# Kernel optimization log

Hardware: AMD Instinct MI355X
Metric: run time of the kernel (lower is better)

The kernel has to match this reference:

```python
import jax, jax.numpy as jnp
import numpy as np

N_AGT = 65536
N_CTX = 65536
E = 400000
D_AGT = 128
D_CTX = 128
EPS = 1e-5


def gn(x, w, b):
    # GroupNorm with num_groups=1 over channel dim of [N, C]
    m = jnp.mean(x, axis=-1, keepdims=True)
    v = jnp.mean((x - m) ** 2, axis=-1, keepdims=True)
    return (x - m) * jax.lax.rsqrt(v + EPS) * w + b


def setup_inputs() -> dict:
    key = jax.random.key(0)
    ks = jax.random.split(key, 24)
    s = 0.05
    inp = {
        "agts": jax.random.normal(ks[0], (N_AGT, D_AGT), jnp.float32),
        "ctx": jax.random.normal(ks[1], (N_CTX, D_CTX), jnp.float32),
        "agt_ctrs": jax.random.normal(ks[2], (N_AGT, 2), jnp.float32),
        "ctx_ctrs": jax.random.normal(ks[3], (N_CTX, 2), jnp.float32),
        "hi": jax.random.randint(ks[4], (E,), 0, N_AGT),
        "wi": jax.random.randint(ks[5], (E,), 0, N_CTX),
        # dist: Linear(2, n_ctx) + bias, ReLU, Linear(n_ctx, n_ctx) GN ng=1
        "dist_w1": jax.random.normal(ks[6], (2, D_CTX), jnp.float32) * s,
        "dist_b1": jnp.zeros((D_CTX,), jnp.float32),
        "dist_w2": jax.random.normal(ks[7], (D_CTX, D_CTX), jnp.float32) * s,
        "dist_gw": jnp.ones((D_CTX,), jnp.float32),
        "dist_gb": jnp.zeros((D_CTX,), jnp.float32),
        # query: Linear(n_agt, n_ctx) GN ng=1
        "q_w": jax.random.normal(ks[8], (D_AGT, D_CTX), jnp.float32) * s,
        "q_gw": jnp.ones((D_CTX,), jnp.float32),
        "q_gb": jnp.zeros((D_CTX,), jnp.float32),
        # ctx: Linear(3*n_ctx, n_agt) GN, then Linear(n_agt, n_agt, bias=False)
        "ctx_w1": jax.random.normal(ks[9], (3 * D_CTX, D_AGT), jnp.float32) * s,
        "ctx_gw": jnp.ones((D_AGT,), jnp.float32),
        "ctx_gb": jnp.zeros((D_AGT,), jnp.float32),
        "ctx_w2": jax.random.normal(ks[10], (D_AGT, D_AGT), jnp.float32) * s,
        # agt: Linear(n_agt, n_agt, bias=False)
        "agt_w": jax.random.normal(ks[11], (D_AGT, D_AGT), jnp.float32) * s,
        # norm: GroupNorm(1, n_agt)
        "norm_w": jnp.ones((D_AGT,), jnp.float32),
        "norm_b": jnp.zeros((D_AGT,), jnp.float32),
        # linear: Linear(n_agt, n_agt) GN, act=False
        "lin_w": jax.random.normal(ks[12], (D_AGT, D_AGT), jnp.float32) * s,
        "lin_gw": jnp.ones((D_AGT,), jnp.float32),
        "lin_gb": jnp.zeros((D_AGT,), jnp.float32),
    }
    return inp


def reference(agts, ctx, agt_ctrs, ctx_ctrs, hi, wi,
              dist_w1, dist_b1, dist_w2, dist_gw, dist_gb,
              q_w, q_gw, q_gb,
              ctx_w1, ctx_gw, ctx_gb, ctx_w2,
              agt_w, norm_w, norm_b,
              lin_w, lin_gw, lin_gb):
    res = agts
    # edge features: relative displacement -> dist MLP
    d = agt_ctrs[hi] - ctx_ctrs[wi]                      # [E, 2]
    d = jax.nn.relu(d @ dist_w1 + dist_b1)               # [E, D_CTX]
    d = jax.nn.relu(gn(d @ dist_w2, dist_gw, dist_gb))
    # query from gathered agent features
    q = jax.nn.relu(gn(agts[hi] @ q_w, q_gw, q_gb))      # [E, D_CTX]
    # gathered context features
    c = ctx[wi]                                          # [E, D_CTX]
    m = jnp.concatenate([d, q, c], axis=1)               # [E, 3*D_CTX]
    m = jax.nn.relu(gn(m @ ctx_w1, ctx_gw, ctx_gb))      # [E, D_AGT]
    m = m @ ctx_w2                                       # [E, D_AGT]
    # aggregate messages back to agents (scatter-add)
    out = agts @ agt_w
    out = out.at[hi].add(m)
    out = jax.nn.relu(gn(out, norm_w, norm_b))
    out = gn(out @ lin_w, lin_gw, lin_gb)                # act=False
    out = jax.nn.relu(out + res)
    return out
```

## Files before the change

kernel.cpp:

```cpp
#include <hip/hip_runtime.h>
#include <hip/hip_bf16.h>

#define TILE_E 32
#define WSTRIDE 132
#define SB 136
#define SF 132
#define FS 16384

#define FRAG_DW2 0
#define FRAG_W1D 1
#define FRAG_CW2 2
#define FRAG_AGT 3
#define FRAG_QW  4
#define FRAG_W1Q 5
#define FRAG_W1C 6
#define FRAG_LIN 7

typedef __attribute__((ext_vector_type(8))) short short8;
typedef __attribute__((ext_vector_type(4))) float f32x4;

__device__ __forceinline__ unsigned short f2bf(float f) {
    union { float f; unsigned u; } v; v.f = f;
    unsigned r = v.u + 0x7fff + ((v.u >> 16) & 1);
    return (unsigned short)(r >> 16);
}

__device__ __forceinline__ float bf2f(unsigned short u) {
    union { unsigned v; float f; } x; x.v = ((unsigned)u) << 16; return x.f;
}

__device__ __forceinline__ f32x4 mfma16(short8 a, short8 b, f32x4 c) {
    return __builtin_amdgcn_mfma_f32_16x16x32_bf16(a, b, c, 0, 0, 0);
}

__device__ __forceinline__ void load_bfrags_fast(const unsigned short* __restrict__ F,
                                                 int wv, int lane, short8 wB[2][4])
{
#pragma unroll
    for (int cb = 0; cb < 2; ++cb)
#pragma unroll
    for (int kc = 0; kc < 4; ++kc)
        wB[cb][kc] = *(const short8*)(F + ((((wv * 2 + cb) * 4 + kc) * 64 + lane) << 3));
}

__device__ __forceinline__ void mfma_gemm32(const unsigned short* __restrict__ X,
                                            const short8 wB[2][4],
                                            f32x4 acc[2][2], int lane)
{
    const int r  = lane & 15;
    const int kg = (lane >> 4) & 3;
#pragma unroll
    for (int rb = 0; rb < 2; ++rb) {
        const unsigned short* xp = X + (rb * 16 + r) * SB + kg * 8;
#pragma unroll
        for (int kc = 0; kc < 4; ++kc) {
            short8 a = *(const short8*)(xp + kc * 32);
            acc[rb][0] = mfma16(a, wB[0][kc], acc[rb][0]);
            acc[rb][1] = mfma16(a, wB[1][kc], acc[rb][1]);
        }
    }
}

__device__ __forceinline__ void gn_row_to_bf16(const float* __restrict__ sY,
                                               const float* __restrict__ gw,
                                               const float* __restrict__ gb,
                                               unsigned short* __restrict__ dst,
                                               int r8, int c0)
{
    const float* yp = sY + r8 * SF + c0;
    float vals[16]; float s1 = 0.f, s2 = 0.f;
#pragma unroll
    for (int i = 0; i < 16; ++i) { float v = yp[i]; vals[i] = v; s1 += v; s2 += v * v; }
#pragma unroll
    for (int off = 4; off >= 1; off >>= 1) {
        s1 += __shfl_xor(s1, off);
        s2 += __shfl_xor(s2, off);
    }
    float m   = s1 * (1.f / 128.f);
    float var = fmaxf(s2 * (1.f / 128.f) - m * m, 0.f);
    float isc = rsqrtf(var + 1e-5f);
    unsigned short* dp = dst + r8 * SB + c0;
#pragma unroll
    for (int i = 0; i < 16; ++i) {
        float y = fmaxf((vals[i] - m) * isc * gw[c0 + i] + gb[c0 + i], 0.f);
        dp[i] = f2bf(y);
    }
}

__device__ __forceinline__ void gn_bf_to_bf16(const unsigned short* __restrict__ sYb,
                                              const float* __restrict__ gw,
                                              const float* __restrict__ gb,
                                              unsigned short* __restrict__ dst,
                                              int r8, int c0)
{
    const unsigned short* yp = sYb + r8 * SB + c0;
    float vals[16]; float s1 = 0.f, s2 = 0.f;
#pragma unroll
    for (int i = 0; i < 16; ++i) { float v = bf2f(yp[i]); vals[i] = v; s1 += v; s2 += v * v; }
#pragma unroll
    for (int off = 4; off >= 1; off >>= 1) {
        s1 += __shfl_xor(s1, off);
        s2 += __shfl_xor(s2, off);
    }
    float m   = s1 * (1.f / 128.f);
    float var = fmaxf(s2 * (1.f / 128.f) - m * m, 0.f);
    float isc = rsqrtf(var + 1e-5f);
    unsigned short* dp = dst + r8 * SB + c0;
#pragma unroll
    for (int i = 0; i < 16; ++i) {
        float y = fmaxf((vals[i] - m) * isc * gw[c0 + i] + gb[c0 + i], 0.f);
        dp[i] = f2bf(y);
    }
}

__global__ __launch_bounds__(256) void prep_hist_kernel(
    const float* __restrict__ W0, const float* __restrict__ W1,
    const float* __restrict__ W2, const float* __restrict__ W3,
    const float* __restrict__ W4, const float* __restrict__ W5,
    const float* __restrict__ W6, const float* __restrict__ W7,
    unsigned short* __restrict__ dst,
    const int* __restrict__ hi, int* __restrict__ hist, int E)
{
    const int b = blockIdx.x;
    if (b < 512) {
        int t = b * 256 + threadIdx.x;
        int m = t >> 14;
        int e = t & (FS - 1);
        int j    = e & 7;
        int lane = (e >> 3) & 63;
        int kc   = (e >> 9) & 3;
        int cb   = (e >> 11) & 1;
        int wv   = (e >> 12) & 3;
        int k = kc * 32 + ((lane >> 4) & 3) * 8 + j;
        int c = wv * 32 + cb * 16 + (lane & 15);
        const float* W = m == 0 ? W0 : m == 1 ? W1 : m == 2 ? W2 : m == 3 ? W3
                       : m == 4 ? W4 : m == 5 ? W5 : m == 6 ? W6 : W7;
        dst[t] = f2bf(W[k * 128 + c]);
    } else {
        for (int i = (b - 512) * 256 + threadIdx.x; i < E; i += 256 * 256)
            atomicAdd(&hist[hi[i]], 1);
    }
}

__device__ __forceinline__ void chunk_sum_body(const int* __restrict__ hist,
                                               int* __restrict__ csum,
                                               int b, int nbins)
{
    __shared__ int red[4];
    int idx = b * 256 + threadIdx.x;
    int v = (idx < nbins) ? hist[idx] : 0;
#pragma unroll
    for (int off = 32; off >= 1; off >>= 1) v += __shfl_xor(v, off);
    if ((threadIdx.x & 63) == 0) red[threadIdx.x >> 6] = v;
    __syncthreads();
    if (threadIdx.x == 0) csum[b] = red[0] + red[1] + red[2] + red[3];
}

__global__ __launch_bounds__(256) void scanB_kernel(const int* __restrict__ csum,
                                                    int* __restrict__ coff, int nchunks)
{
    __shared__ int part[256];
    int t = threadIdx.x;
    int v = (t < nchunks) ? csum[t] : 0;
    part[t] = v;
    __syncthreads();
    for (int off = 1; off < 256; off <<= 1) {
        int p = (t >= off) ? part[t - off] : 0;
        __syncthreads();
        part[t] += p;
        __syncthreads();
    }
    if (t < nchunks) coff[t] = part[t] - v;
}

__global__ __launch_bounds__(256) void scanC_kernel(const int* __restrict__ hist,
                                                    const int* __restrict__ coff,
                                                    int* __restrict__ binCtr, int nbins)
{
    __shared__ int part[256];
    int b = blockIdx.x, t = threadIdx.x;
    int idx = b * 256 + t;
    int v = (idx < nbins) ? hist[idx] : 0;
    part[t] = v;
    __syncthreads();
    for (int off = 1; off < 256; off <<= 1) {
        int p = (t >= off) ? part[t - off] : 0;
        __syncthreads();
        part[t] += p;
        __syncthreads();
    }
    if (idx < nbins) binCtr[idx] = part[t] - v + coff[b];
}

__global__ __launch_bounds__(256) void scatter_kernel(
    const int* __restrict__ hi, const int* __restrict__ wi,
    const float* __restrict__ agt_ctrs, const float* __restrict__ ctx_ctrs,
    int* __restrict__ binCtr,
    int* __restrict__ hiS, int* __restrict__ wiS,
    float* __restrict__ dxS, float* __restrict__ dyS, int E)
{
    for (int i = blockIdx.x * 256 + threadIdx.x; i < E; i += 256 * 256) {
        int h = hi[i], w = wi[i];
        int p = atomicAdd(&binCtr[h], 1);
        hiS[p] = h; wiS[p] = w;
        dxS[p] = agt_ctrs[2 * h]     - ctx_ctrs[2 * w];
        dyS[p] = agt_ctrs[2 * h + 1] - ctx_ctrs[2 * w + 1];
    }
}

__device__ __forceinline__ void kq_tile_body(
    int tile, const float* __restrict__ agts,
    const float* __restrict__ q_gw, const float* __restrict__ q_gb,
    const unsigned short* __restrict__ frags,
    float* __restrict__ qm, int N,
    unsigned short* sX, float* sY, float* sGw, float* sGb)
{
    const int tid  = threadIdx.x;
    const int lane = tid & 63;
    const int wv   = tid >> 6;
    const int colbase = wv * 32;
    const int r8 = tid >> 3, c0 = (tid & 7) * 16;
    const int cl = lane & 15, rq = lane >> 4;

    short8 wBq[2][4], wB1[2][4];
    load_bfrags_fast(frags + FRAG_QW  * FS, wv, lane, wBq);
    load_bfrags_fast(frags + FRAG_W1Q * FS, wv, lane, wB1);
    if (tid < 128) { sGw[tid] = q_gw[tid]; sGb[tid] = q_gb[tid]; }

    const int base = tile * 32;
    {
        int row = base + r8; if (row >= N) row = N - 1;
        const float* src = agts + (size_t)row * 128 + c0;
        short8 v0, v1;
#pragma unroll
        for (int i = 0; i < 8; ++i) { v0[i] = (short)f2bf(src[i]); v1[i] = (short)f2bf(src[i + 8]); }
        short8* dp = (short8*)(sX + r8 * SB + c0);
        dp[0] = v0; dp[1] = v1;
    }
    __syncthreads();

    f32x4 aQ[2][2] = {{{0,0,0,0},{0,0,0,0}},{{0,0,0,0},{0,0,0,0}}};
    mfma_gemm32(sX, wBq, aQ, lane);
    {
#pragma unroll
        for (int rb = 0; rb < 2; ++rb)
#pragma unroll
        for (int cb = 0; cb < 2; ++cb)
#pragma unroll
        for (int q = 0; q < 4; ++q)
            sY[(rb * 16 + rq * 4 + q) * SF + colbase + cb * 16 + cl] = aQ[rb][cb][q];
    }
    __syncthreads();
    gn_row_to_bf16(sY, sGw, sGb, sX, r8, c0);
    __syncthreads();

    f32x4 aM[2][2] = {{{0,0,0,0},{0,0,0,0}},{{0,0,0,0},{0,0,0,0}}};
    mfma_gemm32(sX, wB1, aM, lane);
#pragma unroll
    for (int rb = 0; rb < 2; ++rb)
#pragma unroll
    for (int q = 0; q < 4; ++q) {
        int row = base + rb * 16 + rq * 4 + q;
        if (row < N) {
            float2 v = make_float2(aM[rb][0][q], aM[rb][1][q]);
            *(float2*)(qm + (size_t)row * 128 + colbase + cl * 2) = v;
        }
    }
}

__device__ __forceinline__ void kc_tile_body(
    int tile, const float* __restrict__ ctx,
    const unsigned short* __restrict__ frags,
    float* __restrict__ cm, int N, unsigned short* sX)
{
    const int tid  = threadIdx.x;
    const int lane = tid & 63;
    const int wv   = tid >> 6;
    const int colbase = wv * 32;
    const int r8 = tid >> 3, c0 = (tid & 7) * 16;
    const int cl = lane & 15, rq = lane >> 4;

    short8 wB[2][4];
    load_bfrags_fast(frags + FRAG_W1C * FS, wv, lane, wB);

    const int base = tile * 32;
    {
        int row = base + r8; if (row >= N) row = N - 1;
        const float* src = ctx + (size_t)row * 128 + c0;
        short8 v0, v1;
#pragma unroll
        for (int i = 0; i < 8; ++i) { v0[i] = (short)f2bf(src[i]); v1[i] = (short)f2bf(src[i + 8]); }
        short8* dp = (short8*)(sX + r8 * SB + c0);
        dp[0] = v0; dp[1] = v1;
    }
    __syncthreads();

    f32x4 acc[2][2] = {{{0,0,0,0},{0,0,0,0}},{{0,0,0,0},{0,0,0,0}}};
    mfma_gemm32(sX, wB, acc, lane);
#pragma unroll
    for (int rb = 0; rb < 2; ++rb)
#pragma unroll
    for (int q = 0; q < 4; ++q) {
        int row = base + rb * 16 + rq * 4 + q;
        if (row < N) {
            float2 v = make_float2(acc[rb][0][q], acc[rb][1][q]);
            *(float2*)(cm + (size_t)row * 128 + colbase + cl * 2) = v;
        }
    }
}

__global__ __launch_bounds__(256) void nodes_kernel(
    const int* __restrict__ hist, int* __restrict__ csum,
    const float* __restrict__ agts, const float* __restrict__ ctx,
    const float* __restrict__ q_gw, const float* __restrict__ q_gb,
    const unsigned short* __restrict__ frags,
    float* __restrict__ qm, float* __restrict__ cm,
    int N, int NC, int nchunks, int tilesA)
{
    __shared__ __align__(16) unsigned short sX[32 * SB];
    __shared__ __align__(16) float sY[32 * SF];
    __shared__ float sGw[128], sGb[128];

    const int b = blockIdx.x;
    if (b < nchunks) { chunk_sum_body(hist, csum, b, N); return; }
    int t = b - nchunks;
    if (t < tilesA)
        kq_tile_body(t, agts, q_gw, q_gb, frags, qm, N, sX, sY, sGw, sGb);
    else
        kc_tile_body(t - tilesA, ctx, frags, cm, NC, sX);
}

__global__ __launch_bounds__(256, 3) void edge_sorted_kernel(
    const int* __restrict__ hiS, const int* __restrict__ wiS,
    const float* __restrict__ dxS, const float* __restrict__ dyS,
    const float* __restrict__ dist_w1, const float* __restrict__ dist_b1,
    const float* __restrict__ dist_gw, const float* __restrict__ dist_gb,
    const float* __restrict__ ctx_gw, const float* __restrict__ ctx_gb,
    const unsigned short* __restrict__ frags,
    const float* __restrict__ qm, const float* __restrict__ cm,
    float* __restrict__ msum, int E, int numTiles)
{
    __shared__ __align__(16) unsigned short sH[32 * SB];
    __shared__ __align__(16) unsigned short sYb[32 * SB];
    __shared__ float sW1[3][128];
    __shared__ float sDGw[128], sDGb[128], sCGw[128], sCGb[128];
    __shared__ int sHiA[32], sWiA[32], sKey[33];
    __shared__ float sDx[32], sDy[32];

    const int tid  = threadIdx.x;
    const int lane = tid & 63;
    const int wv   = tid >> 6;
    const int colbase = wv * 32;
    const int r8 = tid >> 3, c0 = (tid & 7) * 16;
    const int cl = lane & 15, rq = lane >> 4;

    short8 wBh[2][4], wBd[2][4];
    load_bfrags_fast(frags + FRAG_DW2 * FS, wv, lane, wBh);
    load_bfrags_fast(frags + FRAG_W1D * FS, wv, lane, wBd);
    if (tid < 128) {
        sW1[0][tid] = dist_w1[tid];
        sW1[1][tid] = dist_w1[128 + tid];
        sW1[2][tid] = dist_b1[tid];
        sDGw[tid] = dist_gw[tid]; sDGb[tid] = dist_gb[tid];
        sCGw[tid] = ctx_gw[tid];  sCGb[tid] = ctx_gb[tid];
    }

    int ph = 0, pw = 0, pkey = -1; float pdx = 0.f, pdy = 0.f;
    if (tid < 32) {
        pkey = -1 - tid;
        int e = blockIdx.x * 32 + tid;
        if (e < E) { ph = hiS[e]; pw = wiS[e]; pkey = ph; pdx = dxS[e]; pdy = dyS[e]; }
    }

    for (int tile = blockIdx.x; tile < numTiles; tile += gridDim.x) {
        __syncthreads();
        if (tid < 32) {
            sHiA[tid] = ph; sWiA[tid] = pw; sKey[tid] = pkey;
            sDx[tid] = pdx; sDy[tid] = pdy;
        }
        __syncthreads();

        if (tid < 32) {
            pkey = -1 - tid; ph = 0; pw = 0; pdx = 0.f; pdy = 0.f;
            int tn = tile + gridDim.x;
            if (tn < numTiles) {
                int e = tn * 32 + tid;
                if (e < E) { ph = hiS[e]; pw = wiS[e]; pkey = ph; pdx = dxS[e]; pdy = dyS[e]; }
            }
        }

        float2 gq[2][4], gc[2][4];
#pragma unroll
        for (int rb = 0; rb < 2; ++rb)
#pragma unroll
        for (int q = 0; q < 4; ++q) {
            int r = rb * 16 + rq * 4 + q;
            gq[rb][q] = *(const float2*)(qm + (size_t)sHiA[r] * 128 + colbase + cl * 2);
            gc[rb][q] = *(const float2*)(cm + (size_t)sWiA[r] * 128 + colbase + cl * 2);
        }

        {
            float dx = sDx[r8], dy = sDy[r8];
            unsigned short* dst = sH + r8 * SB + c0;
#pragma unroll
            for (int i = 0; i < 16; ++i) {
                int c = c0 + i;
                float v = fmaf(dx, sW1[0][c], fmaf(dy, sW1[1][c], sW1[2][c]));
                dst[i] = f2bf(fmaxf(v, 0.f));
            }
        }
        __syncthreads();

        f32x4 acc[2][2] = {{{0,0,0,0},{0,0,0,0}},{{0,0,0,0},{0,0,0,0}}};
        mfma_gemm32(sH, wBh, acc, lane);
        {
#pragma unroll
            for (int rb = 0; rb < 2; ++rb)
#pragma unroll
            for (int cb = 0; cb < 2; ++cb)
#pragma unroll
            for (int q = 0; q < 4; ++q)
                sYb[(rb * 16 + rq * 4 + q) * SB + colbase + cb * 16 + cl] = f2bf(acc[rb][cb][q]);
        }
        __syncthreads();
        gn_bf_to_bf16(sYb, sDGw, sDGb, sH, r8, c0);
        __syncthreads();

        f32x4 a2[2][2];
#pragma unroll
        for (int rb = 0; rb < 2; ++rb)
#pragma unroll
        for (int q = 0; q < 4; ++q) {
            a2[rb][0][q] = gq[rb][q].x + gc[rb][q].x;
            a2[rb][1][q] = gq[rb][q].y + gc[rb][q].y;
        }
        mfma_gemm32(sH, wBd, a2, lane);
        {
#pragma unroll
            for (int rb = 0; rb < 2; ++rb)
#pragma unroll
            for (int cb = 0; cb < 2; ++cb)
#pragma unroll
            for (int q = 0; q < 4; ++q)
                sYb[(rb * 16 + rq * 4 + q) * SB + colbase + cb * 16 + cl] = f2bf(a2[rb][cb][q]);
        }
        __syncthreads();
        gn_bf_to_bf16(sYb, sCGw, sCGb, sH, r8, c0);
        __syncthreads();

        {
            const int col   = tid & 127;
            const int rbase = (tid >> 7) * 16;
            float sum = 0.f;
#pragma unroll
            for (int i = 0; i < 16; ++i) {
                int r = rbase + i;
                sum += bf2f(sH[r * SB + col]);
                bool segEnd = (i == 15) || (sKey[r + 1] != sKey[r]);
                if (segEnd) {
                    int key = sKey[r];
                    if (key >= 0) atomicAdd(&msum[(size_t)key * 128 + col], sum);
                    sum = 0.f;
                }
            }
        }
    }
}

__global__ __launch_bounds__(256) void final_mfma_kernel(
    const float* __restrict__ agts, const float* __restrict__ msum,
    const float* __restrict__ norm_w, const float* __restrict__ norm_b,
    const float* __restrict__ lin_gw, const float* __restrict__ lin_gb,
    const unsigned short* __restrict__ frags,
    float* __restrict__ out, int N)
{
    __shared__ __align__(16) unsigned short sXa[32 * SB];
    __shared__ __align__(16) unsigned short sXm[32 * SB];
    __shared__ float sNw[128], sNb[128], sLw[128], sLb[128];

    const int tid  = threadIdx.x;
    const int lane = tid & 63;
    const int wv   = tid >> 6;
    const int colbase = wv * 32;
    const int r8 = tid >> 3, c0 = (tid & 7) * 16;
    const int cl = lane & 15, rq = lane >> 4;

    short8 wBa[2][4], wB2[2][4], wBl[2][4];
    load_bfrags_fast(frags + FRAG_AGT * FS, wv, lane, wBa);
    load_bfrags_fast(frags + FRAG_CW2 * FS, wv, lane, wB2);
    load_bfrags_fast(frags + FRAG_LIN * FS, wv, lane, wBl);
    if (tid < 128) {
        sNw[tid] = norm_w[tid]; sNb[tid] = norm_b[tid];
        sLw[tid] = lin_gw[tid]; sLb[tid] = lin_gb[tid];
    }

    const int base = blockIdx.x * 32;
    {
        int row = base + r8; if (row >= N) row = N - 1;
        const float* sa = agts + (size_t)row * 128 + c0;
        const float* sm = msum + (size_t)row * 128 + c0;
        short8 a0, a1, m0, m1;
#pragma unroll
        for (int i = 0; i < 8; ++i) {
            a0[i] = (short)f2bf(sa[i]); a1[i] = (short)f2bf(sa[i + 8]);
            m0[i] = (short)f2bf(sm[i]); m1[i] = (short)f2bf(sm[i + 8]);
        }
        short8* da = (short8*)(sXa + r8 * SB + c0);
        short8* dm = (short8*)(sXm + r8 * SB + c0);
        da[0] = a0; da[1] = a1; dm[0] = m0; dm[1] = m1;
    }
    __syncthreads();

    f32x4 acc[2][2] = {{{0,0,0,0},{0,0,0,0}},{{0,0,0,0},{0,0,0,0}}};
    mfma_gemm32(sXa, wBa, acc, lane);
    mfma_gemm32(sXm, wB2, acc, lane);
    __syncthreads();
    {
#pragma unroll
        for (int rb = 0; rb < 2; ++rb)
#pragma unroll
        for (int cb = 0; cb < 2; ++cb)
#pragma unroll
        for (int q = 0; q < 4; ++q)
            sXm[(rb * 16 + rq * 4 + q) * SB + colbase + cb * 16 + cl] = f2bf(acc[rb][cb][q]);
    }
    __syncthreads();
    gn_bf_to_bf16(sXm, sNw, sNb, sXa, r8, c0);
    __syncthreads();

    f32x4 aL[2][2] = {{{0,0,0,0},{0,0,0,0}},{{0,0,0,0},{0,0,0,0}}};
    mfma_gemm32(sXa, wBl, aL, lane);
    __syncthreads();
    {
#pragma unroll
        for (int rb = 0; rb < 2; ++rb)
#pragma unroll
        for (int cb = 0; cb < 2; ++cb)
#pragma unroll
        for (int q = 0; q < 4; ++q)
            sXm[(rb * 16 + rq * 4 + q) * SB + colbase + cb * 16 + cl] = f2bf(aL[rb][cb][q]);
    }
    __syncthreads();
    {
        int row = base + r8;
        if (row < N) {
            const unsigned short* yp = sXm + r8 * SB + c0;
            float vals[16]; float s1 = 0.f, s2 = 0.f;
#pragma unroll
            for (int i = 0; i < 16; ++i) { float v = bf2f(yp[i]); vals[i] = v; s1 += v; s2 += v * v; }
#pragma unroll
            for (int off = 4; off >= 1; off >>= 1) {
                s1 += __shfl_xor(s1, off);
                s2 += __shfl_xor(s2, off);
            }
            float m   = s1 * (1.f / 128.f);
            float var = fmaxf(s2 * (1.f / 128.f) - m * m, 0.f);
            float isc = rsqrtf(var + 1e-5f);
            const float* rp = agts + (size_t)row * 128 + c0;
            float* op = out + (size_t)row * 128 + c0;
#pragma unroll
            for (int i = 0; i < 16; ++i) {
                float y = (vals[i] - m) * isc * sLw[c0 + i] + sLb[c0 + i] + rp[i];
                op[i] = fmaxf(y, 0.f);
            }
        }
    }
}

__device__ __forceinline__ void gemm_tile(const float* __restrict__ sX,
                                          const float* __restrict__ sWT,
                                          int lc, int rg,
                                          float acc0[8], float acc1[8])
{
    const float* w0p = sWT + lc * WSTRIDE;
    const float* w1p = sWT + (lc + 64) * WSTRIDE;
    const float* xp  = sX + rg * 8 * WSTRIDE;
#pragma unroll 4
    for (int k = 0; k < 128; k += 4) {
        float4 w0 = *(const float4*)(w0p + k);
        float4 w1 = *(const float4*)(w1p + k);
#pragma unroll
        for (int j = 0; j < 8; ++j) {
            float4 x = *(const float4*)(xp + j * WSTRIDE + k);
            acc0[j] = fmaf(x.x, w0.x, acc0[j]);
            acc0[j] = fmaf(x.y, w0.y, acc0[j]);
            acc0[j] = fmaf(x.z, w0.z, acc0[j]);
            acc0[j] = fmaf(x.w, w0.w, acc0[j]);
            acc1[j] = fmaf(x.x, w1.x, acc1[j]);
            acc1[j] = fmaf(x.y, w1.y, acc1[j]);
            acc1[j] = fmaf(x.z, w1.z, acc1[j]);
            acc1[j] = fmaf(x.w, w1.w, acc1[j]);
        }
    }
}

__device__ __forceinline__ void stage_wt(const float* __restrict__ W,
                                         float* __restrict__ sWT, int tid)
{
    const int c  = tid & 127;
    const int k0 = tid >> 7;
    float*       dst = sWT + c * WSTRIDE + k0;
    const float* src = W + tid;
    float v[16];
#pragma unroll
    for (int p = 0; p < 4; ++p) {
#pragma unroll
        for (int i = 0; i < 16; ++i) v[i] = src[(p * 16 + i) * 256];
#pragma unroll
        for (int i = 0; i < 16; ++i) dst[(p * 16 + i) * 2] = v[i];
    }
}

__device__ __forceinline__ void gn_rows_lds(const float acc0[8], const float acc1[8],
                                            float gw0, float gw1, float gb0, float gb1,
                                            bool relu, float* __restrict__ dst,
                                            int lc, int rg)
{
#pragma unroll
    for (int j = 0; j < 8; ++j) {
        float s1 = acc0[j] + acc1[j];
        float s2 = acc0[j] * acc0[j] + acc1[j] * acc1[j];
#pragma unroll
        for (int off = 32; off >= 1; off >>= 1) {
            s1 += __shfl_xor(s1, off);
            s2 += __shfl_xor(s2, off);
        }
        float m   = s1 * (1.f / 128.f);
        float var = fmaxf(s2 * (1.f / 128.f) - m * m, 0.f);
        float isc = rsqrtf(var + 1e-5f);
        float y0  = (acc0[j] - m) * isc * gw0 + gb0;
        float y1  = (acc1[j] - m) * isc * gw1 + gb1;
        if (relu) { y0 = fmaxf(y0, 0.f); y1 = fmaxf(y1, 0.f); }
        int r = rg * 8 + j;
        dst[r * WSTRIDE + lc]      = y0;
        dst[r * WSTRIDE + lc + 64] = y1;
    }
}

__global__ __launch_bounds__(256) void rowgemm_kernel(
    const float* __restrict__ X, const float* __restrict__ W,
    float* __restrict__ Y, int n)
{
    __shared__ float sWT[128 * WSTRIDE];
    __shared__ float sX[TILE_E * WSTRIDE];
    const int tid  = threadIdx.x;
    const int base = blockIdx.x * TILE_E;
    {
        int r = tid >> 3, c0 = (tid & 7) * 16;
        int row = base + r;
        if (row < n) {
            const float* src = X + (size_t)row * 128 + c0;
            float*       dst = sX + r * WSTRIDE + c0;
#pragma unroll
            for (int i = 0; i < 4; ++i)
                *(float4*)(dst + i * 4) = *(const float4*)(src + i * 4);
        }
    }
    stage_wt(W, sWT, tid);
    __syncthreads();
    const int lc = tid & 63, rg = tid >> 6;
    float acc0[8] = {0,0,0,0,0,0,0,0}, acc1[8] = {0,0,0,0,0,0,0,0};
    gemm_tile(sX, sWT, lc, rg, acc0, acc1);
#pragma unroll
    for (int j = 0; j < 8; ++j) {
        int row = base + rg * 8 + j;
        if (row < n) {
            Y[(size_t)row * 128 + lc]      = acc0[j];
            Y[(size_t)row * 128 + lc + 64] = acc1[j];
        }
    }
}

__global__ __launch_bounds__(256) void edge_kernel(
    const float* __restrict__ agt_ctrs, const float* __restrict__ ctx_ctrs,
    const int* __restrict__ hi, const int* __restrict__ wi,
    const float* __restrict__ qsrc, const float* __restrict__ ctx,
    const float* __restrict__ dist_w1, const float* __restrict__ dist_b1,
    const float* __restrict__ dist_w2,
    const float* __restrict__ dist_gw, const float* __restrict__ dist_gb,
    const float* __restrict__ q_w,
    const float* __restrict__ q_gw, const float* __restrict__ q_gb,
    const float* __restrict__ ctx_w1,
    const float* __restrict__ ctx_gw, const float* __restrict__ ctx_gb,
    const float* __restrict__ ctx_w2,
    float* __restrict__ out, int E, int numTiles)
{
    __shared__ float sWT[128 * WSTRIDE];
    __shared__ float sH2[TILE_E * WSTRIDE];
    __shared__ float sD2[TILE_E * WSTRIDE];
    __shared__ float sQ2[TILE_E * WSTRIDE];
    __shared__ float sC2[TILE_E * WSTRIDE];
    __shared__ int   sHi[TILE_E];
    __shared__ int   sWiB[TILE_E];
    __shared__ float sDx2[TILE_E], sDy2[TILE_E];

    const int tid = threadIdx.x;
    const int lc = tid & 63, rg = tid >> 6;

    const float dgw0 = dist_gw[lc], dgw1 = dist_gw[lc + 64];
    const float dgb0 = dist_gb[lc], dgb1 = dist_gb[lc + 64];
    const float cgw0 = ctx_gw[lc],  cgw1 = ctx_gw[lc + 64];
    const float cgb0 = ctx_gb[lc],  cgb1 = ctx_gb[lc + 64];
    const float qgw0 = q_gw[lc], qgw1 = q_gw[lc + 64];
    const float qgb0 = q_gb[lc], qgb1 = q_gb[lc + 64];
    const int   hc  = tid & 127;
    const int   hrg = tid >> 7;
    const float w1x = dist_w1[hc], w1y = dist_w1[128 + hc], b1c = dist_b1[hc];

    for (int tile = blockIdx.x; tile < numTiles; tile += gridDim.x) {
        const int base = tile * TILE_E;
        __syncthreads();
        if (tid < TILE_E) {
            int e = base + tid;
            int h = 0, w = 0;
            if (e < E) { h = hi[e]; w = wi[e]; }
            sHi[tid]  = h;
            sWiB[tid] = w;
            sDx2[tid] = agt_ctrs[2 * h]     - ctx_ctrs[2 * w];
            sDy2[tid] = agt_ctrs[2 * h + 1] - ctx_ctrs[2 * w + 1];
        }
        __syncthreads();
        {
            int r = tid >> 3, c0 = (tid & 7) * 16;
            int h = sHi[r], w = sWiB[r];
            const float* qs = qsrc + (size_t)h * 128 + c0;
            const float* cs = ctx  + (size_t)w * 128 + c0;
            float* qd = sQ2 + r * WSTRIDE + c0;
            float* cd = sC2 + r * WSTRIDE + c0;
#pragma unroll
            for (int i = 0; i < 4; ++i) {
                *(float4*)(qd + i * 4) = *(const float4*)(qs + i * 4);
                *(float4*)(cd + i * 4) = *(const float4*)(cs + i * 4);
            }
        }
        {
#pragma unroll
            for (int j = 0; j < 16; ++j) {
                int r = hrg * 16 + j;
                float v = fmaf(sDx2[r], w1x, fmaf(sDy2[r], w1y, b1c));
                sH2[r * WSTRIDE + hc] = fmaxf(v, 0.f);
            }
        }
        __syncthreads();
        stage_wt(q_w, sWT, tid);
        __syncthreads();
        {
            float a0[8] = {0,0,0,0,0,0,0,0}, a1[8] = {0,0,0,0,0,0,0,0};
            gemm_tile(sQ2, sWT, lc, rg, a0, a1);
            __syncthreads();
            gn_rows_lds(a0, a1, qgw0, qgw1, qgb0, qgb1, true, sQ2, lc, rg);
        }
        __syncthreads();
        stage_wt(dist_w2, sWT, tid);
        __syncthreads();
        {
            float a0[8] = {0,0,0,0,0,0,0,0}, a1[8] = {0,0,0,0,0,0,0,0};
            gemm_tile(sH2, sWT, lc, rg, a0, a1);
            gn_rows_lds(a0, a1, dgw0, dgw1, dgb0, dgb1, true, sD2, lc, rg);
        }
        float m0[8] = {0,0,0,0,0,0,0,0}, m1[8] = {0,0,0,0,0,0,0,0};
        __syncthreads();
        stage_wt(ctx_w1, sWT, tid);
        __syncthreads();
        gemm_tile(sD2, sWT, lc, rg, m0, m1);
        __syncthreads();
        stage_wt(ctx_w1 + 128 * 128, sWT, tid);
        __syncthreads();
        gemm_tile(sQ2, sWT, lc, rg, m0, m1);
        __syncthreads();
        stage_wt(ctx_w1 + 2 * 128 * 128, sWT, tid);
        __syncthreads();
        gemm_tile(sC2, sWT, lc, rg, m0, m1);
        gn_rows_lds(m0, m1, cgw0, cgw1, cgb0, cgb1, true, sH2, lc, rg);
        __syncthreads();
        stage_wt(ctx_w2, sWT, tid);
        __syncthreads();
        {
            float a0[8] = {0,0,0,0,0,0,0,0}, a1[8] = {0,0,0,0,0,0,0,0};
            gemm_tile(sH2, sWT, lc, rg, a0, a1);
#pragma unroll
            for (int j = 0; j < 8; ++j) {
                int r = rg * 8 + j;
                int e = base + r;
                if (e < E) {
                    int h = sHi[r];
                    atomicAdd(&out[(size_t)h * 128 + lc],      a0[j]);
                    atomicAdd(&out[(size_t)h * 128 + lc + 64], a1[j]);
                }
            }
        }
    }
}

__global__ __launch_bounds__(256) void final_kernel(
    const float* __restrict__ agts,
    const float* __restrict__ norm_w, const float* __restrict__ norm_b,
    const float* __restrict__ lin_w,
    const float* __restrict__ lin_gw, const float* __restrict__ lin_gb,
    float* __restrict__ out, int n)
{
    __shared__ float sWT[128 * WSTRIDE];
    __shared__ float sX[TILE_E * WSTRIDE];
    const int tid  = threadIdx.x;
    const int base = blockIdx.x * TILE_E;
    {
        int r = tid >> 3, c0 = (tid & 7) * 16;
        int row = base + r;
        if (row < n) {
            const float* src = out + (size_t)row * 128 + c0;
            float vals[16];
            float s1 = 0.f, s2 = 0.f;
#pragma unroll
            for (int i = 0; i < 16; ++i) {
                float v = src[i];
                vals[i] = v; s1 += v; s2 += v * v;
            }
#pragma unroll
            for (int off = 4; off >= 1; off >>= 1) {
                s1 += __shfl_xor(s1, off);
                s2 += __shfl_xor(s2, off);
            }
            float m   = s1 * (1.f / 128.f);
            float var = fmaxf(s2 * (1.f / 128.f) - m * m, 0.f);
            float isc = rsqrtf(var + 1e-5f);
            float* dst = sX + r * WSTRIDE + c0;
#pragma unroll
            for (int i = 0; i < 16; ++i) {
                int c = c0 + i;
                float y = (vals[i] - m) * isc * norm_w[c] + norm_b[c];
                dst[i] = fmaxf(y, 0.f);
            }
        }
    }
    stage_wt(lin_w, sWT, tid);
    __syncthreads();
    const int lc = tid & 63, rg = tid >> 6;
    float acc0[8] = {0,0,0,0,0,0,0,0}, acc1[8] = {0,0,0,0,0,0,0,0};
    gemm_tile(sX, sWT, lc, rg, acc0, acc1);
    const float lgw0 = lin_gw[lc], lgw1 = lin_gw[lc + 64];
    const float lgb0 = lin_gb[lc], lgb1 = lin_gb[lc + 64];
#pragma unroll
    for (int j = 0; j < 8; ++j) {
        float s1 = acc0[j] + acc1[j];
        float s2 = acc0[j] * acc0[j] + acc1[j] * acc1[j];
#pragma unroll
        for (int off = 32; off >= 1; off >>= 1) {
            s1 += __shfl_xor(s1, off);
            s2 += __shfl_xor(s2, off);
        }
        float m   = s1 * (1.f / 128.f);
        float var = fmaxf(s2 * (1.f / 128.f) - m * m, 0.f);
        float isc = rsqrtf(var + 1e-5f);
        int row = base + rg * 8 + j;
        if (row < n) {
            size_t ro = (size_t)row * 128;
            float y0 = (acc0[j] - m) * isc * lgw0 + lgb0 + agts[ro + lc];
            float y1 = (acc1[j] - m) * isc * lgw1 + lgb1 + agts[ro + lc + 64];
            out[ro + lc]      = fmaxf(y0, 0.f);
            out[ro + lc + 64] = fmaxf(y1, 0.f);
        }
    }
}

extern "C" void kernel_launch(void* const* d_in, const int* in_sizes, int n_in,
                              void* d_out, int out_size, void* d_ws, size_t ws_size,
                              hipStream_t stream)
{
    const float* agts     = (const float*)d_in[0];
    const float* ctx      = (const float*)d_in[1];
    const float* agt_ctrs = (const float*)d_in[2];
    const float* ctx_ctrs = (const float*)d_in[3];
    const int*   hi       = (const int*)d_in[4];
    const int*   wi       = (const int*)d_in[5];
    const float* dist_w1  = (const float*)d_in[6];
    const float* dist_b1  = (const float*)d_in[7];
    const float* dist_w2  = (const float*)d_in[8];
    const float* dist_gw  = (const float*)d_in[9];
    const float* dist_gb  = (const float*)d_in[10];
    const float* q_w      = (const float*)d_in[11];
    const float* q_gw     = (const float*)d_in[12];
    const float* q_gb     = (const float*)d_in[13];
    const float* ctx_w1   = (const float*)d_in[14];
    const float* ctx_gw   = (const float*)d_in[15];
    const float* ctx_gb   = (const float*)d_in[16];
    const float* ctx_w2   = (const float*)d_in[17];
    const float* agt_w    = (const float*)d_in[18];
    const float* norm_w   = (const float*)d_in[19];
    const float* norm_b   = (const float*)d_in[20];
    const float* lin_w    = (const float*)d_in[21];
    const float* lin_gw   = (const float*)d_in[22];
    const float* lin_gb   = (const float*)d_in[23];

    const int N  = in_sizes[0] / 128;
    const int NC = in_sizes[1] / 128;
    const int E  = in_sizes[4];
    float* out = (float*)d_out;

    const int tilesA   = (N + 31) / 32;
    const int tilesC   = (NC + 31) / 32;
    const int numTiles = (E + 31) / 32;
    const int nchunks  = (N + 255) / 256;

    const size_t needQM = (size_t)N  * 128 * sizeof(float);
    const size_t needCM = (size_t)NC * 128 * sizeof(float);
    const size_t needMS = (size_t)N  * 128 * sizeof(float);
    const size_t needH  = (size_t)N * sizeof(int);
    const size_t needB  = (size_t)N * sizeof(int);
    const size_t needE4 = (size_t)E * sizeof(int);
    const size_t needF  = (size_t)8 * FS * sizeof(unsigned short);
    const size_t needSc = 512 * sizeof(int);
    const size_t needTotal = needQM + needCM + needMS + needH + needB
                           + 4 * needE4 + needF + needSc;

    if (ws_size >= needTotal && nchunks <= 256) {
        char* w = (char*)d_ws;
        float*          qm     = (float*)w;            w += needQM;
        float*          cm     = (float*)w;            w += needCM;
        float*          msum   = (float*)w;            w += needMS;
        int*            hist   = (int*)w;              w += needH;
        int*            binCtr = (int*)w;              w += needB;
        int*            hiS    = (int*)w;              w += needE4;
        int*            wiS    = (int*)w;              w += needE4;
        float*          dxS    = (float*)w;            w += needE4;
        float*          dyS    = (float*)w;            w += needE4;
        int*            csum   = (int*)w;              w += 256 * sizeof(int);
        int*            coff   = (int*)w;              w += 256 * sizeof(int);
        unsigned short* fragsW = (unsigned short*)w;   w += needF;

        hipMemsetAsync(msum, 0, needMS + needH, stream);

        prep_hist_kernel<<<768, 256, 0, stream>>>(
            dist_w2, ctx_w1, ctx_w2, agt_w, q_w,
            ctx_w1 + 128 * 128, ctx_w1 + 2 * 128 * 128, lin_w, fragsW,
            hi, hist, E);

        nodes_kernel<<<nchunks + tilesA + tilesC, 256, 0, stream>>>(
            hist, csum, agts, ctx, q_gw, q_gb, fragsW, qm, cm,
            N, NC, nchunks, tilesA);

        scanB_kernel<<<1, 256, 0, stream>>>(csum, coff, nchunks);
        scanC_kernel<<<nchunks, 256, 0, stream>>>(hist, coff, binCtr, N);

        scatter_kernel<<<256, 256, 0, stream>>>(hi, wi, agt_ctrs, ctx_ctrs,
            binCtr, hiS, wiS, dxS, dyS, E);

        int gridE = numTiles < 2048 ? numTiles : 2048;
        edge_sorted_kernel<<<gridE, 256, 0, stream>>>(
            hiS, wiS, dxS, dyS,
            dist_w1, dist_b1, dist_gw, dist_gb, ctx_gw, ctx_gb,
            fragsW, qm, cm, msum, E, numTiles);

        final_mfma_kernel<<<tilesA, 256, 0, stream>>>(
            agts, msum, norm_w, norm_b, lin_gw, lin_gb, fragsW, out, N);
    } else {
        rowgemm_kernel<<<tilesA, 256, 0, stream>>>(agts, agt_w, out, N);
        int gridE = numTiles < 8192 ? numTiles : 8192;
        edge_kernel<<<gridE, 256, 0, stream>>>(agt_ctrs, ctx_ctrs, hi, wi,
            agts, ctx,
            dist_w1, dist_b1, dist_w2, dist_gw, dist_gb,
            q_w, q_gw, q_gb,
            ctx_w1, ctx_gw, ctx_gb, ctx_w2,
            out, E, numTiles);
        final_kernel<<<tilesA, 256, 0, stream>>>(agts, norm_w, norm_b,
            lin_w, lin_gw, lin_gb, out, N);
    }
}
```

Baseline: 230.2 us.

## Fuse scan stages, overlap edge scatter with node GEMMs, vectorize LDS stores

The three-kernel scan becomes two: a chunk-sum kernel, then one kernel where each block adds its own preceding chunk sums. The edge counting-sort scatter moves into nodes_kernel as extra blocks, so it runs alongside the query and context node GEMM tiles instead of as a separate launch. GroupNorm and dist-MLP LDS reads and writes now use 16-byte vector accesses. The edge kernel occupancy hint rises from 3 to 4 blocks, which may add register pressure or spills.

```diff
diff --git a/kernel.cpp b/kernel.cpp
--- a/kernel.cpp
+++ b/kernel.cpp
@@ -61,30 +61,44 @@
     }
 }
 
+__device__ __forceinline__ void gn_core_pack(float vals[16],
+                                             const float* __restrict__ gw,
+                                             const float* __restrict__ gb,
+                                             int c0, short8& o0, short8& o1)
+{
+    float s1 = 0.f, s2 = 0.f;
+#pragma unroll
+    for (int i = 0; i < 16; ++i) { s1 += vals[i]; s2 += vals[i] * vals[i]; }
+#pragma unroll
+    for (int off = 4; off >= 1; off >>= 1) {
+        s1 += __shfl_xor(s1, off);
+        s2 += __shfl_xor(s2, off);
+    }
+    float m   = s1 * (1.f / 128.f);
+    float var = fmaxf(s2 * (1.f / 128.f) - m * m, 0.f);
+    float isc = rsqrtf(var + 1e-5f);
+#pragma unroll
+    for (int i = 0; i < 16; ++i) {
+        float y = fmaxf((vals[i] - m) * isc * gw[c0 + i] + gb[c0 + i], 0.f);
+        unsigned short u = f2bf(y);
+        if (i < 8) o0[i] = (short)u; else o1[i - 8] = (short)u;
+    }
+}
+
 __device__ __forceinline__ void gn_row_to_bf16(const float* __restrict__ sY,
                                                const float* __restrict__ gw,
                                                const float* __restrict__ gb,
                                                unsigned short* __restrict__ dst,
                                                int r8, int c0)
 {
-    const float* yp = sY + r8 * SF + c0;
-    float vals[16]; float s1 = 0.f, s2 = 0.f;
-#pragma unroll
-    for (int i = 0; i < 16; ++i) { float v = yp[i]; vals[i] = v; s1 += v; s2 += v * v; }
-#pragma unroll
-    for (int off = 4; off >= 1; off >>= 1) {
-        s1 += __shfl_xor(s1, off);
-        s2 += __shfl_xor(s2, off);
-    }
-    float m   = s1 * (1.f / 128.f);
-    float var = fmaxf(s2 * (1.f / 128.f) - m * m, 0.f);
-    float isc = rsqrtf(var + 1e-5f);
-    unsigned short* dp = dst + r8 * SB + c0;
-#pragma unroll
-    for (int i = 0; i < 16; ++i) {
-        float y = fmaxf((vals[i] - m) * isc * gw[c0 + i] + gb[c0 + i], 0.f);
-        dp[i] = f2bf(y);
-    }
+    const float4* yv = (const float4*)(sY + r8 * SF + c0);
+    float4 a = yv[0], b = yv[1], c = yv[2], d = yv[3];
+    float vals[16] = { a.x,a.y,a.z,a.w, b.x,b.y,b.z,b.w,
+                       c.x,c.y,c.z,c.w, d.x,d.y,d.z,d.w };
+    short8 o0, o1;
+    gn_core_pack(vals, gw, gb, c0, o0, o1);
+    short8* dp = (short8*)(dst + r8 * SB + c0);
+    dp[0] = o0; dp[1] = o1;
 }
 
 __device__ __forceinline__ void gn_bf_to_bf16(const unsigned short* __restrict__ sYb,
@@ -93,24 +107,18 @@
                                               unsigned short* __restrict__ dst,
                                               int r8, int c0)
 {
-    const unsigned short* yp = sYb + r8 * SB + c0;
-    float vals[16]; float s1 = 0.f, s2 = 0.f;
-#pragma unroll
-    for (int i = 0; i < 16; ++i) { float v = bf2f(yp[i]); vals[i] = v; s1 += v; s2 += v * v; }
-#pragma unroll
-    for (int off = 4; off >= 1; off >>= 1) {
-        s1 += __shfl_xor(s1, off);
-        s2 += __shfl_xor(s2, off);
-    }
-    float m   = s1 * (1.f / 128.f);
-    float var = fmaxf(s2 * (1.f / 128.f) - m * m, 0.f);
-    float isc = rsqrtf(var + 1e-5f);
-    unsigned short* dp = dst + r8 * SB + c0;
-#pragma unroll
-    for (int i = 0; i < 16; ++i) {
-        float y = fmaxf((vals[i] - m) * isc * gw[c0 + i] + gb[c0 + i], 0.f);
-        dp[i] = f2bf(y);
-    }
+    const short8* yv = (const short8*)(sYb + r8 * SB + c0);
+    short8 a = yv[0], b = yv[1];
+    float vals[16];
+#pragma unroll
+    for (int i = 0; i < 8; ++i) {
+        vals[i]     = bf2f((unsigned short)a[i]);
+        vals[8 + i] = bf2f((unsigned short)b[i]);
+    }
+    short8 o0, o1;
+    gn_core_pack(vals, gw, gb, c0, o0, o1);
+    short8* dp = (short8*)(dst + r8 * SB + c0);
+    dp[0] = o0; dp[1] = o1;
 }
 
 __global__ __launch_bounds__(256) void prep_hist_kernel(
@@ -142,11 +150,11 @@
     }
 }
 
-__device__ __forceinline__ void chunk_sum_body(const int* __restrict__ hist,
-                                               int* __restrict__ csum,
-                                               int b, int nbins)
+__global__ __launch_bounds__(256) void scanA_kernel(const int* __restrict__ hist,
+                                                    int* __restrict__ csum, int nbins)
 {
     __shared__ int red[4];
+    int b = blockIdx.x;
     int idx = b * 256 + threadIdx.x;
     int v = (idx < nbins) ? hist[idx] : 0;
 #pragma unroll
@@ -156,29 +164,23 @@
     if (threadIdx.x == 0) csum[b] = red[0] + red[1] + red[2] + red[3];
 }
 
-__global__ __launch_bounds__(256) void scanB_kernel(const int* __restrict__ csum,
-                                                    int* __restrict__ coff, int nchunks)
+__global__ __launch_bounds__(256) void scanBC_kernel(const int* __restrict__ hist,
+                                                     const int* __restrict__ csum,
+                                                     int* __restrict__ binCtr,
+                                                     int nbins, int nchunks)
 {
     __shared__ int part[256];
-    int t = threadIdx.x;
-    int v = (t < nchunks) ? csum[t] : 0;
-    part[t] = v;
-    __syncthreads();
-    for (int off = 1; off < 256; off <<= 1) {
-        int p = (t >= off) ? part[t - off] : 0;
-        __syncthreads();
-        part[t] += p;
-        __syncthreads();
-    }
-    if (t < nchunks) coff[t] = part[t] - v;
-}
-
-__global__ __launch_bounds__(256) void scanC_kernel(const int* __restrict__ hist,
-                                                    const int* __restrict__ coff,
-                                                    int* __restrict__ binCtr, int nbins)
-{
-    __shared__ int part[256];
-    int b = blockIdx.x, t = threadIdx.x;
+    __shared__ int red[4];
+    __shared__ int coffb;
+    const int b = blockIdx.x, t = threadIdx.x;
+
+    int cv = (t < b && t < nchunks) ? csum[t] : 0;
+#pragma unroll
+    for (int off = 32; off >= 1; off >>= 1) cv += __shfl_xor(cv, off);
+    if ((t & 63) == 0) red[t >> 6] = cv;
+    __syncthreads();
+    if (t == 0) coffb = red[0] + red[1] + red[2] + red[3];
+
     int idx = b * 256 + t;
     int v = (idx < nbins) ? hist[idx] : 0;
     part[t] = v;
@@ -189,23 +191,7 @@
         part[t] += p;
         __syncthreads();
     }
-    if (idx < nbins) binCtr[idx] = part[t] - v + coff[b];
-}
-
-__global__ __launch_bounds__(256) void scatter_kernel(
-    const int* __restrict__ hi, const int* __restrict__ wi,
-    const float* __restrict__ agt_ctrs, const float* __restrict__ ctx_ctrs,
-    int* __restrict__ binCtr,
-    int* __restrict__ hiS, int* __restrict__ wiS,
-    float* __restrict__ dxS, float* __restrict__ dyS, int E)
-{
-    for (int i = blockIdx.x * 256 + threadIdx.x; i < E; i += 256 * 256) {
-        int h = hi[i], w = wi[i];
-        int p = atomicAdd(&binCtr[h], 1);
-        hiS[p] = h; wiS[p] = w;
-        dxS[p] = agt_ctrs[2 * h]     - ctx_ctrs[2 * w];
-        dyS[p] = agt_ctrs[2 * h + 1] - ctx_ctrs[2 * w + 1];
-    }
+    if (idx < nbins) binCtr[idx] = part[t] - v + coffb;
 }
 
 __device__ __forceinline__ void kq_tile_body(
@@ -310,27 +296,40 @@
 }
 
 __global__ __launch_bounds__(256) void nodes_kernel(
-    const int* __restrict__ hist, int* __restrict__ csum,
+    const int* __restrict__ hi, const int* __restrict__ wi,
+    const float* __restrict__ agt_ctrs, const float* __restrict__ ctx_ctrs,
+    int* __restrict__ binCtr,
+    int* __restrict__ hiS, int* __restrict__ wiS,
+    float* __restrict__ dxS, float* __restrict__ dyS,
     const float* __restrict__ agts, const float* __restrict__ ctx,
     const float* __restrict__ q_gw, const float* __restrict__ q_gb,
     const unsigned short* __restrict__ frags,
     float* __restrict__ qm, float* __restrict__ cm,
-    int N, int NC, int nchunks, int tilesA)
+    int E, int N, int NC, int tilesA)
 {
     __shared__ __align__(16) unsigned short sX[32 * SB];
     __shared__ __align__(16) float sY[32 * SF];
     __shared__ float sGw[128], sGb[128];
 
     const int b = blockIdx.x;
-    if (b < nchunks) { chunk_sum_body(hist, csum, b, N); return; }
-    int t = b - nchunks;
+    if (b < 256) {
+        for (int i = b * 256 + threadIdx.x; i < E; i += 256 * 256) {
+            int h = hi[i], w = wi[i];
+            int p = atomicAdd(&binCtr[h], 1);
+            hiS[p] = h; wiS[p] = w;
+            dxS[p] = agt_ctrs[2 * h]     - ctx_ctrs[2 * w];
+            dyS[p] = agt_ctrs[2 * h + 1] - ctx_ctrs[2 * w + 1];
+        }
+        return;
+    }
+    int t = b - 256;
     if (t < tilesA)
         kq_tile_body(t, agts, q_gw, q_gb, frags, qm, N, sX, sY, sGw, sGb);
     else
         kc_tile_body(t - tilesA, ctx, frags, cm, NC, sX);
 }
 
-__global__ __launch_bounds__(256, 3) void edge_sorted_kernel(
+__global__ __launch_bounds__(256, 4) void edge_sorted_kernel(
     const int* __restrict__ hiS, const int* __restrict__ wiS,
     const float* __restrict__ dxS, const float* __restrict__ dyS,
     const float* __restrict__ dist_w1, const float* __restrict__ dist_b1,
@@ -401,13 +400,16 @@
 
         {
             float dx = sDx[r8], dy = sDy[r8];
-            unsigned short* dst = sH + r8 * SB + c0;
+            short8 o0, o1;
 #pragma unroll
             for (int i = 0; i < 16; ++i) {
                 int c = c0 + i;
                 float v = fmaf(dx, sW1[0][c], fmaf(dy, sW1[1][c], sW1[2][c]));
-                dst[i] = f2bf(fmaxf(v, 0.f));
-            }
+                unsigned short u = f2bf(fmaxf(v, 0.f));
+                if (i < 8) o0[i] = (short)u; else o1[i - 8] = (short)u;
+            }
+            short8* dp = (short8*)(sH + r8 * SB + c0);
+            dp[0] = o0; dp[1] = o1;
         }
         __syncthreads();
 
@@ -544,10 +546,16 @@
     {
         int row = base + r8;
         if (row < N) {
-            const unsigned short* yp = sXm + r8 * SB + c0;
+            const short8* yv = (const short8*)(sXm + r8 * SB + c0);
+            short8 a = yv[0], b = yv[1];
             float vals[16]; float s1 = 0.f, s2 = 0.f;
 #pragma unroll
-            for (int i = 0; i < 16; ++i) { float v = bf2f(yp[i]); vals[i] = v; s1 += v; s2 += v * v; }
+            for (int i = 0; i < 8; ++i) {
+                vals[i]     = bf2f((unsigned short)a[i]);
+                vals[8 + i] = bf2f((unsigned short)b[i]);
+            }
+#pragma unroll
+            for (int i = 0; i < 16; ++i) { s1 += vals[i]; s2 += vals[i] * vals[i]; }
 #pragma unroll
             for (int off = 4; off >= 1; off >>= 1) {
                 s1 += __shfl_xor(s1, off);
@@ -923,8 +931,7 @@
         int*            wiS    = (int*)w;              w += needE4;
         float*          dxS    = (float*)w;            w += needE4;
         float*          dyS    = (float*)w;            w += needE4;
-        int*            csum   = (int*)w;              w += 256 * sizeof(int);
-        int*            coff   = (int*)w;              w += 256 * sizeof(int);
+        int*            csum   = (int*)w;              w += 512 * sizeof(int);
         unsigned short* fragsW = (unsigned short*)w;   w += needF;
 
         hipMemsetAsync(msum, 0, needMS + needH, stream);
@@ -934,15 +941,13 @@
             ctx_w1 + 128 * 128, ctx_w1 + 2 * 128 * 128, lin_w, fragsW,
             hi, hist, E);
 
-        nodes_kernel<<<nchunks + tilesA + tilesC, 256, 0, stream>>>(
-            hist, csum, agts, ctx, q_gw, q_gb, fragsW, qm, cm,
-            N, NC, nchunks, tilesA);
-
-        scanB_kernel<<<1, 256, 0, stream>>>(csum, coff, nchunks);
-        scanC_kernel<<<nchunks, 256, 0, stream>>>(hist, coff, binCtr, N);
-
-        scatter_kernel<<<256, 256, 0, stream>>>(hi, wi, agt_ctrs, ctx_ctrs,
-            binCtr, hiS, wiS, dxS, dyS, E);
+        scanA_kernel<<<nchunks, 256, 0, stream>>>(hist, csum, N);
+        scanBC_kernel<<<nchunks, 256, 0, stream>>>(hist, csum, binCtr, N, nchunks);
+
+        nodes_kernel<<<256 + tilesA + tilesC, 256, 0, stream>>>(
+            hi, wi, agt_ctrs, ctx_ctrs, binCtr, hiS, wiS, dxS, dyS,
+            agts, ctx, q_gw, q_gb, fragsW, qm, cm,
+            E, N, NC, tilesA);
 
         int gridE = numTiles < 2048 ? numTiles : 2048;
         edge_sorted_kernel<<<gridE, 256, 0, stream>>>(
```

Measured after the change: 302.8 us. 31.5% more time.
